# Optimization experiments

Hardware: AMD Instinct MI355X
Metric: run time of the kernel (lower is better)

The kernel has to match this reference:

```python
import jax, jax.numpy as jnp
import numpy as np

BS, P, R, D = 32, 128, 16, 1024
RHO = 0.97
EPS = 1e-8


def unit_normalize(x):
    return x / jnp.maximum(jnp.linalg.norm(x, axis=-1, keepdims=True), EPS)


def setup_inputs() -> dict:
    key = jax.random.key(0)
    ks = jax.random.split(key, 12)
    scale = 1.0 / np.sqrt(D)
    return {
        "x_all": jax.random.normal(ks[0], (BS, P, D), jnp.float32),
        "h_all": jax.random.normal(ks[1], (BS, P, D), jnp.float32),
        "surprise_all": jax.random.uniform(ks[2], (BS, P, 1), jnp.float32) * 8.0,
        "reset_mask": jax.random.bernoulli(ks[3], 0.05, (BS, P)),
        "pm_K": unit_normalize(jax.random.normal(ks[4], (BS, R, D), jnp.float32)),
        "pm_V": unit_normalize(jax.random.normal(ks[5], (BS, R, D), jnp.float32)),
        "pm_a": jax.random.uniform(ks[6], (BS, R), jnp.float32),
        "elig_K0": jnp.zeros((BS, R, D), jnp.float32),
        "elig_V0": jnp.zeros((BS, R, D), jnp.float32),
        "W_k": jax.random.normal(ks[7], (D, D), jnp.float32) * scale,
        "b_k": jnp.zeros((D,), jnp.float32),
        "W_v": jax.random.normal(ks[8], (D, D), jnp.float32) * scale,
        "b_v": jnp.zeros((D,), jnp.float32),
    }


def reference(x_all, h_all, surprise_all, reset_mask, pm_K, pm_V, pm_a,
              elig_K0, elig_V0, W_k, b_k, W_v, b_v):
    # ---- apply_batch: read-only slot-memory readout over P tokens ----
    x_q = unit_normalize(x_all)                                  # [BS,P,D]
    scores = jnp.einsum('brd,bpd->bpr', pm_K, x_q)               # [BS,P,R]
    weighted = pm_a[:, None, :] * scores                         # [BS,P,R]
    y_pm = jnp.einsum('bpr,brd->bpd', weighted, pm_V)            # [BS,P,D]

    # ---- update_eligibility_batch: affine scan over P tokens ----
    k_cand = unit_normalize(jnp.einsum('bpd,de->bpe', x_all, W_k) + b_k)  # [BS,P,D]
    v_cand = jnp.einsum('bpd,de->bpe', h_all, W_v) + b_v                  # [BS,P,D]
    gate = jnp.clip(surprise_all[..., 0] / 5.0, 0.0, 1.0)                 # [BS,P]
    a_keep = RHO * (1.0 - reset_mask.astype(jnp.float32))                 # [BS,P]

    def step(carry, inp):
        eK, eV = carry                      # each [BS,R,D]
        k, v, g, a = inp                    # [BS,D],[BS,D],[BS],[BS]
        # b_t = gate * cand, broadcast across the R slots (matches torch expand)
        eK = a[:, None, None] * eK + (g[:, None] * k)[:, None, :]
        eV = a[:, None, None] * eV + (g[:, None] * v)[:, None, :]
        return (eK, eV), None

    xs = (jnp.swapaxes(k_cand, 0, 1), jnp.swapaxes(v_cand, 0, 1),
          gate.T, a_keep.T)                 # leading axis = P
    (elig_K, elig_V), _ = jax.lax.scan(step, (elig_K0, elig_V0), xs)

    return y_pm, elig_K, elig_V
```

## Files before the change

kernel.cpp:

```cpp
#include <hip/hip_runtime.h>
#include <cstdint>
#include <cstddef>

#define NB 32
#define NP 128
#define NR 16
#define ND 1024
#define RHOC 0.97f
#define EPSN 1e-8f

typedef short bf16x8 __attribute__((ext_vector_type(8)));
typedef float f32x4 __attribute__((ext_vector_type(4)));
typedef unsigned short u16x8 __attribute__((ext_vector_type(8)));
typedef unsigned short ushort_t;

__device__ inline ushort_t f2bf(float f) {
  unsigned u = __float_as_uint(f);
  unsigned r = (u + 0x7fffu + ((u >> 16) & 1u)) >> 16;
  return (ushort_t)r;
}
__device__ inline float bf2f(ushort_t v) {
  return __uint_as_float(((unsigned)v) << 16);
}
__device__ inline void gload16(const void* g, void* l) {
  __builtin_amdgcn_global_load_lds(
      (const __attribute__((address_space(1))) void*)g,
      (__attribute__((address_space(3))) void*)l, 16, 0, 0);
}

__global__ __launch_bounds__(256) void prep_kernel(
    const float* __restrict__ surprise, const void* __restrict__ mask,
    const float* __restrict__ x, const float* __restrict__ Wk,
    const float* __restrict__ pmK,
    float* __restrict__ c, float* __restrict__ Abuf, float* __restrict__ csum,
    ushort_t* __restrict__ Xb, float* __restrict__ xnorm,
    ushort_t* __restrict__ WkT, ushort_t* __restrict__ pmKb) {
  __shared__ __align__(16) char smem[8448];
  int bid = blockIdx.x;
  int t = threadIdx.x;
  if (bid < NB) {
    float* a_sh = (float*)smem;
    float* suf  = a_sh + 128;
    float* redc = suf + 129;
    int*   isu8 = (int*)(redc + 128);
    int b = bid;
    if (t == 0) *isu8 = 0;
    __syncthreads();
    const unsigned char* mb = (const unsigned char*)mask;
    int v = 0;
    for (int i = t; i < NB * NP; i += 256)
      if ((i & 3) != 0 && mb[i] != 0) v = 1;
    if (v) *isu8 = 1;
    __syncthreads();
    int u8 = *isu8;
    if (t < NP) {
      int mv = u8 ? mb[b * NP + t] : ((const int*)mask)[b * NP + t];
      a_sh[t] = RHOC * (mv ? 0.f : 1.f);
    }
    __syncthreads();
    if (t == 0) {
      float p = 1.f;
      suf[NP] = 1.f;
      for (int s = NP - 1; s >= 0; --s) { p *= a_sh[s]; suf[s] = p; }
    }
    __syncthreads();
    if (t < NP) {
      float g = fminf(fmaxf(surprise[b * NP + t] * 0.2f, 0.f), 1.f);
      float cv = g * suf[t + 1];
      c[b * NP + t] = cv;
      redc[t] = cv;
    }
    __syncthreads();
    for (int off = 64; off > 0; off >>= 1) {
      if (t < off) redc[t] += redc[t + off];
      __syncthreads();
    }
    if (t == 0) { csum[b] = redc[0]; Abuf[b] = suf[0]; }
  } else if (bid < NB + NB * NP) {
    int row = bid - NB;
    float* red = (float*)smem;
    float4 vv = *(const float4*)&x[(size_t)row * ND + t * 4];
    ushort4 o;
    o.x = f2bf(vv.x); o.y = f2bf(vv.y); o.z = f2bf(vv.z); o.w = f2bf(vv.w);
    *(ushort4*)&Xb[(size_t)row * ND + t * 4] = o;
    float ss = vv.x * vv.x + vv.y * vv.y + vv.z * vv.z + vv.w * vv.w;
#pragma unroll
    for (int off = 32; off > 0; off >>= 1) ss += __shfl_xor(ss, off);
    int wave = t >> 6, lane = t & 63;
    if (lane == 0) red[wave] = ss;
    __syncthreads();
    if (t == 0) xnorm[row] = sqrtf(red[0] + red[1] + red[2] + red[3]);
  } else if (bid < NB + NB * NP + 256) {
    int id2 = bid - (NB + NB * NP);
    ushort_t (*tt)[65] = (ushort_t(*)[65])smem;
    int k0 = (id2 >> 4) * 64, n0 = (id2 & 15) * 64;
#pragma unroll
    for (int i = 0; i < 16; ++i) {
      int r = i * 4 + (t >> 6), cc = t & 63;
      tt[r][cc] = f2bf(Wk[(size_t)(k0 + r) * ND + n0 + cc]);
    }
    __syncthreads();
#pragma unroll
    for (int i = 0; i < 16; ++i) {
      int r = i * 4 + (t >> 6), cc = t & 63;
      WkT[(size_t)(n0 + r) * ND + k0 + cc] = tt[cc][r];
    }
  } else {
    int id3 = bid - (NB + NB * NP + 256);
    size_t base = (size_t)id3 * 2048 + t * 8;
    float4 a = *(const float4*)&pmK[base];
    float4 bq = *(const float4*)&pmK[base + 4];
    u16x8 o;
    o[0] = f2bf(a.x); o[1] = f2bf(a.y); o[2] = f2bf(a.z); o[3] = f2bf(a.w);
    o[4] = f2bf(bq.x); o[5] = f2bf(bq.y); o[6] = f2bf(bq.z); o[7] = f2bf(bq.w);
    *(u16x8*)&pmKb[base] = o;
  }
}

__global__ __launch_bounds__(256, 3) void main_kernel(
    const ushort_t* __restrict__ Xb, const ushort_t* __restrict__ WkT,
    const float* __restrict__ bk, float* __restrict__ norms2p,
    const float* __restrict__ h, const float* __restrict__ c,
    float* __restrict__ hbar) {
  __shared__ __align__(16) char smem[50176];
  int bid = blockIdx.x;
  int tid = threadIdx.x;
  int grp = bid >> 3, sub = bid & 7;
  int id = (grp >> 1) * 8 + sub;
  if ((grp & 1) == 0) {
    ushort_t* As = (ushort_t*)smem;
    ushort_t* Bs = As + 2 * 128 * 64;
    float* sred = (float*)(Bs + 2 * 64 * 64);
    int lane = tid & 63, wid = tid >> 6;
    int wr = wid >> 1, wc = wid & 1;
    int bm = id & 31, bn = id >> 5;
    int m0 = bm * 128, n0 = bn * 64;
    int lo = lane & 15, hi = lane >> 4;
    f32x4 acc[4][2] = {};

    int ra = tid >> 1, sa = (tid & 1) * 4;
#define STAGE(buf, k0)                                                        \
  {                                                                           \
    _Pragma("unroll") for (int i = 0; i < 4; ++i) {                           \
      int sl = i * 256 + tid;                                                 \
      int r = sl >> 3, s = sl & 7;                                            \
      int gk = (k0) + ((s ^ (r & 7)) << 3);                                   \
      gload16(&Xb[(size_t)(m0 + r) * ND + gk],                                \
              &As[(size_t)(buf)*8192 + ((size_t)sl << 3)]);                   \
    }                                                                         \
    _Pragma("unroll") for (int i = 0; i < 2; ++i) {                           \
      int sl = i * 256 + tid;                                                 \
      int r = sl >> 3, s = sl & 7;                                            \
      int gk = (k0) + ((s ^ (r & 7)) << 3);                                   \
      gload16(&WkT[(size_t)(n0 + r) * ND + gk],                               \
              &Bs[(size_t)(buf)*4096 + ((size_t)sl << 3)]);                   \
    }                                                                         \
  }

    STAGE(0, 0);
    __syncthreads();
    int cur = 0;
    for (int t = 0; t < 16; ++t) {
      if (t < 15) STAGE(cur ^ 1, (t + 1) * 64);
      const ushort_t* Ab = As + cur * 8192;
      const ushort_t* Bb = Bs + cur * 4096;
#pragma unroll
      for (int ksl = 0; ksl < 2; ++ksl) {
        bf16x8 af[4], bfr[2];
#pragma unroll
        for (int mi = 0; mi < 4; ++mi) {
          int r = wr * 64 + mi * 16 + lo;
          int s = (ksl * 4 + hi) ^ (r & 7);
          af[mi] = *(const bf16x8*)&Ab[(r << 6) + (s << 3)];
        }
#pragma unroll
        for (int ni = 0; ni < 2; ++ni) {
          int r = wc * 32 + ni * 16 + lo;
          int s = (ksl * 4 + hi) ^ (r & 7);
          bfr[ni] = *(const bf16x8*)&Bb[(r << 6) + (s << 3)];
        }
#pragma unroll
        for (int mi = 0; mi < 4; ++mi)
#pragma unroll
          for (int ni = 0; ni < 2; ++ni)
            acc[mi][ni] = __builtin_amdgcn_mfma_f32_16x16x32_bf16(
                af[mi], bfr[ni], acc[mi][ni], 0, 0, 0);
      }
      __syncthreads();
      cur ^= 1;
    }
#undef STAGE
    float bkv[2];
#pragma unroll
    for (int ni = 0; ni < 2; ++ni) bkv[ni] = bk[n0 + wc * 32 + ni * 16 + lo];
#pragma unroll
    for (int mi = 0; mi < 4; ++mi) {
#pragma unroll
      for (int j = 0; j < 4; ++j) {
        float ss = 0.f;
#pragma unroll
        for (int ni = 0; ni < 2; ++ni) {
          float vv = acc[mi][ni][j] + bkv[ni];
          ss += vv * vv;
        }
        ss += __shfl_xor(ss, 1);
        ss += __shfl_xor(ss, 2);
        ss += __shfl_xor(ss, 4);
        ss += __shfl_xor(ss, 8);
        if (lo == 0) sred[wc * 128 + wr * 64 + mi * 16 + hi * 4 + j] = ss;
      }
    }
    __syncthreads();
    if (tid < 128)
      norms2p[(size_t)bn * (NB * NP) + m0 + tid] = sred[tid] + sred[128 + tid];
  } else {
    int b = id >> 4, dchunk = id & 15;
    float* cs = (float*)smem;
    float* red = cs + 128;
    int dd = tid & 63, sl = tid >> 6;
    int d = dchunk * 64 + dd;
    if (tid < NP) cs[tid] = c[b * NP + tid];
    __syncthreads();
    const float* hb = h + ((size_t)b * NP + sl * 32) * ND + d;
    float acc = 0.f;
#pragma unroll
    for (int tt2 = 0; tt2 < 32; ++tt2) acc += cs[sl * 32 + tt2] * hb[(size_t)tt2 * ND];
    red[sl * 64 + dd] = acc;
    __syncthreads();
    if (sl == 0)
      hbar[(size_t)b * ND + d] = red[dd] + red[64 + dd] + red[128 + dd] + red[192 + dd];
  }
}

__global__ __launch_bounds__(256) void mid_kernel(
    const ushort_t* __restrict__ Xb, const float* __restrict__ norms2p,
    const float* __restrict__ c, float* __restrict__ xbar,
    float* __restrict__ wsum, const ushort_t* __restrict__ pmKb,
    const float* __restrict__ pmV, const float* __restrict__ pma,
    const float* __restrict__ xnorm, float* __restrict__ y) {
  __shared__ __align__(16) char smem[5504];
  int bid = blockIdx.x;
  int tid = threadIdx.x;
  int grp = bid >> 3, sub = bid & 7;
  int id = (grp >> 1) * 8 + sub;
  if ((grp & 1) == 0) {
    float* wsh = (float*)smem;
    float* red = wsh + NP;
    int b = id >> 3;
    int dd = tid & 63, sl = tid >> 6;
    int d = (id & 7) * 128 + dd * 2;
    if (tid < NP) {
      float s = 0.f;
#pragma unroll
      for (int pc = 0; pc < 16; ++pc)
        s += norms2p[(size_t)pc * (NB * NP) + b * NP + tid];
      wsh[tid] = c[b * NP + tid] / fmaxf(sqrtf(s), EPSN);
    }
    __syncthreads();
    if ((id & 7) == 0 && tid == 0) {
      float s = 0.f;
      for (int t2 = 0; t2 < NP; ++t2) s += wsh[t2];
      wsum[b] = s;
    }
    const ushort_t* xb = Xb + ((size_t)b * NP + sl * 32) * ND + d;
    float ax = 0.f, ay = 0.f;
#pragma unroll
    for (int t2 = 0; t2 < 32; ++t2) {
      unsigned u = *(const unsigned*)&xb[(size_t)t2 * ND];
      float w = wsh[sl * 32 + t2];
      ax += w * bf2f((ushort_t)(u & 0xffffu));
      ay += w * bf2f((ushort_t)(u >> 16));
    }
    red[(sl * 64 + dd) * 2 + 0] = ax;
    red[(sl * 64 + dd) * 2 + 1] = ay;
    __syncthreads();
    if (sl == 0) {
      float2 o;
      o.x = red[dd * 2] + red[(64 + dd) * 2] + red[(128 + dd) * 2] + red[(192 + dd) * 2];
      o.y = red[dd * 2 + 1] + red[(64 + dd) * 2 + 1] + red[(128 + dd) * 2 + 1] +
            red[(192 + dd) * 2 + 1];
      *(float2*)&xbar[(size_t)b * ND + d] = o;
    }
  } else {
    int b = id >> 3, p0 = (id & 7) * 16;
    float* sredp = (float*)smem;
    float* wls = sredp + 4 * 16 * 17;
    int lane = tid & 63, wid = tid >> 6;
    int lo = lane & 15, hi = lane >> 4;
    float4 v[16];
#pragma unroll
    for (int r = 0; r < 16; ++r)
      v[r] = *(const float4*)&pmV[((size_t)(b * NR + r)) * ND + tid * 4];
    const ushort_t* xrow = &Xb[((size_t)(b * NP + p0 + lo)) * ND];
    const ushort_t* krow = &pmKb[((size_t)(b * NR + lo)) * ND];
    f32x4 sc = {};
#pragma unroll
    for (int ki = 0; ki < 8; ++ki) {
      int koff = (wid * 8 + ki) * 32 + hi * 8;
      bf16x8 af = *(const bf16x8*)&xrow[koff];
      bf16x8 bf = *(const bf16x8*)&krow[koff];
      sc = __builtin_amdgcn_mfma_f32_16x16x32_bf16(af, bf, sc, 0, 0, 0);
    }
#pragma unroll
    for (int j = 0; j < 4; ++j) sredp[(wid * 16 + hi * 4 + j) * 17 + lo] = sc[j];
    __syncthreads();
    {
      int p = tid >> 4, r = tid & 15;
      float s = sredp[(p)*17 + r] + sredp[(16 + p) * 17 + r] +
                sredp[(32 + p) * 17 + r] + sredp[(48 + p) * 17 + r];
      wls[p * 16 + r] = pma[b * NR + r] * s / fmaxf(xnorm[b * NP + p0 + p], EPSN);
    }
    __syncthreads();
#pragma unroll
    for (int p = 0; p < 16; ++p) {
      float4 a = {0.f, 0.f, 0.f, 0.f};
#pragma unroll
      for (int r = 0; r < 16; ++r) {
        float w = wls[p * 16 + r];
        a.x += w * v[r].x; a.y += w * v[r].y;
        a.z += w * v[r].z; a.w += w * v[r].w;
      }
      *(float4*)&y[((size_t)(b * NP + p0 + p)) * ND + tid * 4] = a;
    }
  }
}

__global__ __launch_bounds__(256) void vkbar_kernel(
    const float* __restrict__ hbar, const float* __restrict__ xbar,
    const float* __restrict__ Wv, const float* __restrict__ Wk,
    float* __restrict__ partials) {
  __shared__ __align__(16) float hst[128][36];
  int bid = blockIdx.x;
  int path = bid >> 7;
  int id2 = bid & 127;
  int esl = id2 >> 4, dchunk = id2 & 15;
  int e0 = esl * 128, d0 = dchunk * 64;
  const float* src = path ? xbar : hbar;
  const float* W = path ? Wk : Wv;
  int t = threadIdx.x;
#pragma unroll
  for (int i = 0; i < 16; ++i) {
    int idx = i * 256 + t;
    int bb = idx >> 7, e = idx & 127;
    hst[e][bb] = src[(size_t)bb * ND + e0 + e];
  }
  __syncthreads();
  int bg = t >> 6, dd = t & 63, d = d0 + dd;
  float acc[8] = {};
  for (int e = 0; e < 128; ++e) {
    float w = W[(size_t)(e0 + e) * ND + d];
    float4 h0 = *(const float4*)&hst[e][bg * 8];
    float4 h1 = *(const float4*)&hst[e][bg * 8 + 4];
    acc[0] += h0.x * w; acc[1] += h0.y * w; acc[2] += h0.z * w; acc[3] += h0.w * w;
    acc[4] += h1.x * w; acc[5] += h1.y * w; acc[6] += h1.z * w; acc[7] += h1.w * w;
  }
#pragma unroll
  for (int i = 0; i < 8; ++i)
    partials[((size_t)(path * 8 + esl) * NB + bg * 8 + i) * ND + d] = acc[i];
}

__global__ __launch_bounds__(256) void epi_kernel(
    const float* __restrict__ partials, const float* __restrict__ bv,
    const float* __restrict__ bk, const float* __restrict__ eV0,
    const float* __restrict__ eK0, const float* __restrict__ Abuf,
    const float* __restrict__ csum, const float* __restrict__ wsum,
    float* __restrict__ outV, float* __restrict__ outK) {
  int bid = blockIdx.x;
  int path = bid >> 7;
  int id2 = bid & 127;
  int b = id2 >> 2, dc = id2 & 3;
  int d = dc * 256 + threadIdx.x;
  float s = 0.f;
#pragma unroll
  for (int sl = 0; sl < 8; ++sl)
    s += partials[((size_t)(path * 8 + sl) * NB + b) * ND + d];
  const float* bias = path ? bk : bv;
  const float* coef = path ? wsum : csum;
  const float* e0p = path ? eK0 : eV0;
  float* out = path ? outK : outV;
  s += coef[b] * bias[d];
  float A = Abuf[b];
#pragma unroll
  for (int r = 0; r < NR; ++r) {
    size_t idx = ((size_t)(b * NR + r)) * ND + d;
    out[idx] = A * e0p[idx] + s;
  }
}

extern "C" void kernel_launch(void* const* d_in, const int* in_sizes, int n_in,
                              void* d_out, int out_size, void* d_ws, size_t ws_size,
                              hipStream_t stream) {
  (void)in_sizes; (void)n_in; (void)out_size; (void)ws_size;
  const float* x_all    = (const float*)d_in[0];
  const float* h_all    = (const float*)d_in[1];
  const float* surprise = (const float*)d_in[2];
  const void*  mask     = d_in[3];
  const float* pmK      = (const float*)d_in[4];
  const float* pmV      = (const float*)d_in[5];
  const float* pma      = (const float*)d_in[6];
  const float* eK0      = (const float*)d_in[7];
  const float* eV0      = (const float*)d_in[8];
  const float* Wk       = (const float*)d_in[9];
  const float* bk       = (const float*)d_in[10];
  const float* Wv       = (const float*)d_in[11];
  const float* bv       = (const float*)d_in[12];

  float* y    = (float*)d_out;
  float* outK = y + (size_t)NB * NP * ND;
  float* outV = outK + (size_t)NB * NR * ND;

  char* w = (char*)d_ws;
  float* c        = (float*)w; w += NB * NP * 4;
  float* Abuf     = (float*)w; w += 256;
  float* csum     = (float*)w; w += 256;
  float* wsum     = (float*)w; w += 256;
  float* hbar     = (float*)w; w += NB * ND * 4;
  float* xbar     = (float*)w; w += NB * ND * 4;
  float* norms2p  = (float*)w; w += (size_t)16 * NB * NP * 4;
  float* xnorm    = (float*)w; w += NB * NP * 4;
  float* partials = (float*)w; w += (size_t)16 * NB * ND * 4;
  ushort_t* WkT   = (ushort_t*)w; w += (size_t)ND * ND * 2;
  ushort_t* pmKb  = (ushort_t*)w; w += (size_t)NB * NR * ND * 2;
  ushort_t* Xb    = (ushort_t*)w; w += (size_t)NB * NP * ND * 2;

  prep_kernel<<<NB + NB * NP + 256 + 256, 256, 0, stream>>>(
      surprise, mask, x_all, Wk, pmK, c, Abuf, csum, Xb, xnorm, WkT, pmKb);
  main_kernel<<<512 + 512, 256, 0, stream>>>(Xb, WkT, bk, norms2p, h_all, c, hbar);
  mid_kernel<<<256 + 256, 256, 0, stream>>>(Xb, norms2p, c, xbar, wsum, pmKb,
                                            pmV, pma, xnorm, y);
  vkbar_kernel<<<256, 256, 0, stream>>>(hbar, xbar, Wv, Wk, partials);
  epi_kernel<<<256, 256, 0, stream>>>(partials, bv, bk, eV0, eK0, Abuf, csum,
                                      wsum, outV, outK);
}
```

Baseline: 66.69 us.

## Reschedule work across kernels and fuse matvec with eligibility epilogue

The hbar reduction (c-weighted sum of h) moves into prep_kernel, and each of its blocks recomputes the decay suffix products locally. The y readout moves into main_kernel alongside the Wk GEMM. The Wv/Wk matvecs are fused with the eligibility epilogue into d3/d4 kernels, which drops the partials buffer and one launch. The aim is better load balance and fewer launches and global round trips, at the cost of redundant mask/suffix work per block and a less parallel matvec (2 batches per block over the full e range).

```diff
diff --git a/kernel.cpp b/kernel.cpp
--- a/kernel.cpp
+++ b/kernel.cpp
@@ -31,22 +31,23 @@
 __global__ __launch_bounds__(256) void prep_kernel(
     const float* __restrict__ surprise, const void* __restrict__ mask,
     const float* __restrict__ x, const float* __restrict__ Wk,
-    const float* __restrict__ pmK,
+    const float* __restrict__ pmK, const float* __restrict__ h,
     float* __restrict__ c, float* __restrict__ Abuf, float* __restrict__ csum,
     ushort_t* __restrict__ Xb, float* __restrict__ xnorm,
-    ushort_t* __restrict__ WkT, ushort_t* __restrict__ pmKb) {
+    ushort_t* __restrict__ WkT, ushort_t* __restrict__ pmKb,
+    float* __restrict__ hbar) {
   __shared__ __align__(16) char smem[8448];
   int bid = blockIdx.x;
   int t = threadIdx.x;
+  const unsigned char* mb = (const unsigned char*)mask;
   if (bid < NB) {
     float* a_sh = (float*)smem;
     float* suf  = a_sh + 128;
-    float* redc = suf + 129;
+    float* redc = suf + 132;
     int*   isu8 = (int*)(redc + 128);
     int b = bid;
     if (t == 0) *isu8 = 0;
     __syncthreads();
-    const unsigned char* mb = (const unsigned char*)mask;
     int v = 0;
     for (int i = t; i < NB * NP; i += 256)
       if ((i & 3) != 0 && mb[i] != 0) v = 1;
@@ -76,8 +77,51 @@
       __syncthreads();
     }
     if (t == 0) { csum[b] = redc[0]; Abuf[b] = suf[0]; }
-  } else if (bid < NB + NB * NP) {
-    int row = bid - NB;
+  } else if (bid < NB + 512) {
+    int id = bid - NB;
+    int b = id >> 4, dchunk = id & 15;
+    float* asw = (float*)smem;
+    float* suf = asw + 128;
+    float* cs  = suf + 132;
+    float* red = cs + 128;
+    int* isu8  = (int*)(red + 256);
+    if (t == 0) *isu8 = 0;
+    __syncthreads();
+    int v = 0;
+    for (int i = t; i < NB * NP; i += 256)
+      if ((i & 3) != 0 && mb[i] != 0) v = 1;
+    if (v) *isu8 = 1;
+    __syncthreads();
+    int u8 = *isu8;
+    if (t < NP) {
+      int mv = u8 ? mb[b * NP + t] : ((const int*)mask)[b * NP + t];
+      asw[t] = RHOC * (mv ? 0.f : 1.f);
+    }
+    __syncthreads();
+    if (t == 0) {
+      float p = 1.f;
+      suf[NP] = 1.f;
+      for (int s = NP - 1; s >= 0; --s) { p *= asw[s]; suf[s] = p; }
+    }
+    __syncthreads();
+    if (t < NP) {
+      float g = fminf(fmaxf(surprise[b * NP + t] * 0.2f, 0.f), 1.f);
+      cs[t] = g * suf[t + 1];
+    }
+    __syncthreads();
+    int dd = t & 63, sl = t >> 6;
+    int d = dchunk * 64 + dd;
+    const float* hb = h + ((size_t)b * NP + sl * 32) * ND + d;
+    float acc = 0.f;
+#pragma unroll
+    for (int tt2 = 0; tt2 < 32; ++tt2)
+      acc += cs[sl * 32 + tt2] * hb[(size_t)tt2 * ND];
+    red[sl * 64 + dd] = acc;
+    __syncthreads();
+    if (sl == 0)
+      hbar[(size_t)b * ND + d] = red[dd] + red[64 + dd] + red[128 + dd] + red[192 + dd];
+  } else if (bid < NB + 512 + NB * NP) {
+    int row = bid - (NB + 512);
     float* red = (float*)smem;
     float4 vv = *(const float4*)&x[(size_t)row * ND + t * 4];
     ushort4 o;
@@ -90,8 +134,8 @@
     if (lane == 0) red[wave] = ss;
     __syncthreads();
     if (t == 0) xnorm[row] = sqrtf(red[0] + red[1] + red[2] + red[3]);
-  } else if (bid < NB + NB * NP + 256) {
-    int id2 = bid - (NB + NB * NP);
+  } else if (bid < NB + 512 + NB * NP + 256) {
+    int id2 = bid - (NB + 512 + NB * NP);
     ushort_t (*tt)[65] = (ushort_t(*)[65])smem;
     int k0 = (id2 >> 4) * 64, n0 = (id2 & 15) * 64;
 #pragma unroll
@@ -106,7 +150,7 @@
       WkT[(size_t)(n0 + r) * ND + k0 + cc] = tt[cc][r];
     }
   } else {
-    int id3 = bid - (NB + NB * NP + 256);
+    int id3 = bid - (NB + 512 + NB * NP + 256);
     size_t base = (size_t)id3 * 2048 + t * 8;
     float4 a = *(const float4*)&pmK[base];
     float4 bq = *(const float4*)&pmK[base + 4];
@@ -120,25 +164,23 @@
 __global__ __launch_bounds__(256, 3) void main_kernel(
     const ushort_t* __restrict__ Xb, const ushort_t* __restrict__ WkT,
     const float* __restrict__ bk, float* __restrict__ norms2p,
-    const float* __restrict__ h, const float* __restrict__ c,
-    float* __restrict__ hbar) {
+    const ushort_t* __restrict__ pmKb, const float* __restrict__ pmV,
+    const float* __restrict__ pma, const float* __restrict__ xnorm,
+    float* __restrict__ y) {
   __shared__ __align__(16) char smem[50176];
   int bid = blockIdx.x;
   int tid = threadIdx.x;
-  int grp = bid >> 3, sub = bid & 7;
-  int id = (grp >> 1) * 8 + sub;
-  if ((grp & 1) == 0) {
+  if (bid < 512) {
     ushort_t* As = (ushort_t*)smem;
     ushort_t* Bs = As + 2 * 128 * 64;
     float* sred = (float*)(Bs + 2 * 64 * 64);
     int lane = tid & 63, wid = tid >> 6;
     int wr = wid >> 1, wc = wid & 1;
-    int bm = id & 31, bn = id >> 5;
+    int bm = bid & 31, bn = bid >> 5;
     int m0 = bm * 128, n0 = bn * 64;
     int lo = lane & 15, hi = lane >> 4;
     f32x4 acc[4][2] = {};
 
-    int ra = tid >> 1, sa = (tid & 1) * 4;
 #define STAGE(buf, k0)                                                        \
   {                                                                           \
     _Pragma("unroll") for (int i = 0; i < 4; ++i) {                           \
@@ -214,36 +256,109 @@
     if (tid < 128)
       norms2p[(size_t)bn * (NB * NP) + m0 + tid] = sred[tid] + sred[128 + tid];
   } else {
-    int b = id >> 4, dchunk = id & 15;
-    float* cs = (float*)smem;
-    float* red = cs + 128;
-    int dd = tid & 63, sl = tid >> 6;
-    int d = dchunk * 64 + dd;
-    if (tid < NP) cs[tid] = c[b * NP + tid];
-    __syncthreads();
-    const float* hb = h + ((size_t)b * NP + sl * 32) * ND + d;
-    float acc = 0.f;
-#pragma unroll
-    for (int tt2 = 0; tt2 < 32; ++tt2) acc += cs[sl * 32 + tt2] * hb[(size_t)tt2 * ND];
-    red[sl * 64 + dd] = acc;
-    __syncthreads();
-    if (sl == 0)
-      hbar[(size_t)b * ND + d] = red[dd] + red[64 + dd] + red[128 + dd] + red[192 + dd];
-  }
-}
-
-__global__ __launch_bounds__(256) void mid_kernel(
+    int id2 = bid - 512;
+    int b = id2 >> 3, p0 = (id2 & 7) * 16;
+    float* sredp = (float*)smem;
+    float* wls = sredp + 4 * 16 * 17;
+    int lane = tid & 63, wid = tid >> 6;
+    int lo = lane & 15, hi = lane >> 4;
+    float4 v[16];
+#pragma unroll
+    for (int r = 0; r < 16; ++r)
+      v[r] = *(const float4*)&pmV[((size_t)(b * NR + r)) * ND + tid * 4];
+    const ushort_t* xrow = &Xb[((size_t)(b * NP + p0 + lo)) * ND];
+    const ushort_t* krow = &pmKb[((size_t)(b * NR + lo)) * ND];
+    f32x4 sc = {};
+#pragma unroll
+    for (int ki = 0; ki < 8; ++ki) {
+      int koff = (wid * 8 + ki) * 32 + hi * 8;
+      bf16x8 af = *(const bf16x8*)&xrow[koff];
+      bf16x8 bf = *(const bf16x8*)&krow[koff];
+      sc = __builtin_amdgcn_mfma_f32_16x16x32_bf16(af, bf, sc, 0, 0, 0);
+    }
+#pragma unroll
+    for (int j = 0; j < 4; ++j) sredp[(wid * 16 + hi * 4 + j) * 17 + lo] = sc[j];
+    __syncthreads();
+    {
+      int p = tid >> 4, r = tid & 15;
+      float s = sredp[(p)*17 + r] + sredp[(16 + p) * 17 + r] +
+                sredp[(32 + p) * 17 + r] + sredp[(48 + p) * 17 + r];
+      wls[p * 16 + r] = pma[b * NR + r] * s / fmaxf(xnorm[b * NP + p0 + p], EPSN);
+    }
+    __syncthreads();
+#pragma unroll
+    for (int p = 0; p < 16; ++p) {
+      float4 a = {0.f, 0.f, 0.f, 0.f};
+#pragma unroll
+      for (int r = 0; r < 16; ++r) {
+        float w = wls[p * 16 + r];
+        a.x += w * v[r].x; a.y += w * v[r].y;
+        a.z += w * v[r].z; a.w += w * v[r].w;
+      }
+      *(float4*)&y[((size_t)(b * NP + p0 + p)) * ND + tid * 4] = a;
+    }
+  }
+}
+
+__device__ __forceinline__ void eligout_body(
+    int id, int tid, const float* __restrict__ src, const float* __restrict__ W,
+    const float* __restrict__ bias, const float* __restrict__ coef,
+    const float* __restrict__ e0, const float* __restrict__ Abuf,
+    float* __restrict__ out, char* smemv) {
+  int bg = id >> 4, dchunk = id & 15;
+  int b0 = bg * 2;
+  float* hs = (float*)smemv;
+  float* red = hs + 2 * ND;
+  for (int i = tid; i < 2 * ND; i += 256) {
+    int bb = i >> 10, e = i & 1023;
+    hs[bb * ND + e] = src[(size_t)(b0 + bb) * ND + e];
+  }
+  __syncthreads();
+  int esl = tid >> 6, dd = tid & 63;
+  int d = dchunk * 64 + dd;
+  float a0 = 0.f, a1 = 0.f;
+  const float* wcol = W + d;
+#pragma unroll 8
+  for (int ei = 0; ei < 256; ++ei) {
+    int e = esl * 256 + ei;
+    float w = wcol[(size_t)e * ND];
+    a0 += hs[e] * w;
+    a1 += hs[ND + e] * w;
+  }
+  red[(esl * 64 + dd) * 2 + 0] = a0;
+  red[(esl * 64 + dd) * 2 + 1] = a1;
+  __syncthreads();
+  if (tid < 128) {
+    int bb = tid >> 6, dd2 = tid & 63;
+    int d2 = dchunk * 64 + dd2;
+    float s = red[dd2 * 2 + bb] + red[(64 + dd2) * 2 + bb] +
+              red[(128 + dd2) * 2 + bb] + red[(192 + dd2) * 2 + bb];
+    int b = b0 + bb;
+    s += coef[b] * bias[d2];
+    float A = Abuf[b];
+#pragma unroll
+    for (int r = 0; r < NR; ++r) {
+      size_t idx = ((size_t)(b * NR + r)) * ND + d2;
+      out[idx] = A * e0[idx] + s;
+    }
+  }
+}
+
+__global__ __launch_bounds__(256) void d3_kernel(
+    const float* __restrict__ hbar, const float* __restrict__ Wv,
+    const float* __restrict__ bv, const float* __restrict__ csum,
+    const float* __restrict__ eV0, const float* __restrict__ Abuf,
+    float* __restrict__ outV,
     const ushort_t* __restrict__ Xb, const float* __restrict__ norms2p,
     const float* __restrict__ c, float* __restrict__ xbar,
-    float* __restrict__ wsum, const ushort_t* __restrict__ pmKb,
-    const float* __restrict__ pmV, const float* __restrict__ pma,
-    const float* __restrict__ xnorm, float* __restrict__ y) {
-  __shared__ __align__(16) char smem[5504];
+    float* __restrict__ wsum) {
+  __shared__ __align__(16) char smem[10240];
   int bid = blockIdx.x;
   int tid = threadIdx.x;
-  int grp = bid >> 3, sub = bid & 7;
-  int id = (grp >> 1) * 8 + sub;
-  if ((grp & 1) == 0) {
+  if (bid < 256) {
+    eligout_body(bid, tid, hbar, Wv, bv, csum, eV0, Abuf, outV, smem);
+  } else {
+    int id = bid - 256;
     float* wsh = (float*)smem;
     float* red = wsh + NP;
     int b = id >> 3;
@@ -281,110 +396,16 @@
             red[(192 + dd) * 2 + 1];
       *(float2*)&xbar[(size_t)b * ND + d] = o;
     }
-  } else {
-    int b = id >> 3, p0 = (id & 7) * 16;
-    float* sredp = (float*)smem;
-    float* wls = sredp + 4 * 16 * 17;
-    int lane = tid & 63, wid = tid >> 6;
-    int lo = lane & 15, hi = lane >> 4;
-    float4 v[16];
-#pragma unroll
-    for (int r = 0; r < 16; ++r)
-      v[r] = *(const float4*)&pmV[((size_t)(b * NR + r)) * ND + tid * 4];
-    const ushort_t* xrow = &Xb[((size_t)(b * NP + p0 + lo)) * ND];
-    const ushort_t* krow = &pmKb[((size_t)(b * NR + lo)) * ND];
-    f32x4 sc = {};
-#pragma unroll
-    for (int ki = 0; ki < 8; ++ki) {
-      int koff = (wid * 8 + ki) * 32 + hi * 8;
-      bf16x8 af = *(const bf16x8*)&xrow[koff];
-      bf16x8 bf = *(const bf16x8*)&krow[koff];
-      sc = __builtin_amdgcn_mfma_f32_16x16x32_bf16(af, bf, sc, 0, 0, 0);
-    }
-#pragma unroll
-    for (int j = 0; j < 4; ++j) sredp[(wid * 16 + hi * 4 + j) * 17 + lo] = sc[j];
-    __syncthreads();
-    {
-      int p = tid >> 4, r = tid & 15;
-      float s = sredp[(p)*17 + r] + sredp[(16 + p) * 17 + r] +
-                sredp[(32 + p) * 17 + r] + sredp[(48 + p) * 17 + r];
-      wls[p * 16 + r] = pma[b * NR + r] * s / fmaxf(xnorm[b * NP + p0 + p], EPSN);
-    }
-    __syncthreads();
-#pragma unroll
-    for (int p = 0; p < 16; ++p) {
-      float4 a = {0.f, 0.f, 0.f, 0.f};
-#pragma unroll
-      for (int r = 0; r < 16; ++r) {
-        float w = wls[p * 16 + r];
-        a.x += w * v[r].x; a.y += w * v[r].y;
-        a.z += w * v[r].z; a.w += w * v[r].w;
-      }
-      *(float4*)&y[((size_t)(b * NP + p0 + p)) * ND + tid * 4] = a;
-    }
-  }
-}
-
-__global__ __launch_bounds__(256) void vkbar_kernel(
-    const float* __restrict__ hbar, const float* __restrict__ xbar,
-    const float* __restrict__ Wv, const float* __restrict__ Wk,
-    float* __restrict__ partials) {
-  __shared__ __align__(16) float hst[128][36];
-  int bid = blockIdx.x;
-  int path = bid >> 7;
-  int id2 = bid & 127;
-  int esl = id2 >> 4, dchunk = id2 & 15;
-  int e0 = esl * 128, d0 = dchunk * 64;
-  const float* src = path ? xbar : hbar;
-  const float* W = path ? Wk : Wv;
-  int t = threadIdx.x;
-#pragma unroll
-  for (int i = 0; i < 16; ++i) {
-    int idx = i * 256 + t;
-    int bb = idx >> 7, e = idx & 127;
-    hst[e][bb] = src[(size_t)bb * ND + e0 + e];
-  }
-  __syncthreads();
-  int bg = t >> 6, dd = t & 63, d = d0 + dd;
-  float acc[8] = {};
-  for (int e = 0; e < 128; ++e) {
-    float w = W[(size_t)(e0 + e) * ND + d];
-    float4 h0 = *(const float4*)&hst[e][bg * 8];
-    float4 h1 = *(const float4*)&hst[e][bg * 8 + 4];
-    acc[0] += h0.x * w; acc[1] += h0.y * w; acc[2] += h0.z * w; acc[3] += h0.w * w;
-    acc[4] += h1.x * w; acc[5] += h1.y * w; acc[6] += h1.z * w; acc[7] += h1.w * w;
-  }
-#pragma unroll
-  for (int i = 0; i < 8; ++i)
-    partials[((size_t)(path * 8 + esl) * NB + bg * 8 + i) * ND + d] = acc[i];
-}
-
-__global__ __launch_bounds__(256) void epi_kernel(
-    const float* __restrict__ partials, const float* __restrict__ bv,
-    const float* __restrict__ bk, const float* __restrict__ eV0,
+  }
+}
+
+__global__ __launch_bounds__(256) void d4_kernel(
+    const float* __restrict__ xbar, const float* __restrict__ Wk,
+    const float* __restrict__ bk, const float* __restrict__ wsum,
     const float* __restrict__ eK0, const float* __restrict__ Abuf,
-    const float* __restrict__ csum, const float* __restrict__ wsum,
-    float* __restrict__ outV, float* __restrict__ outK) {
-  int bid = blockIdx.x;
-  int path = bid >> 7;
-  int id2 = bid & 127;
-  int b = id2 >> 2, dc = id2 & 3;
-  int d = dc * 256 + threadIdx.x;
-  float s = 0.f;
-#pragma unroll
-  for (int sl = 0; sl < 8; ++sl)
-    s += partials[((size_t)(path * 8 + sl) * NB + b) * ND + d];
-  const float* bias = path ? bk : bv;
-  const float* coef = path ? wsum : csum;
-  const float* e0p = path ? eK0 : eV0;
-  float* out = path ? outK : outV;
-  s += coef[b] * bias[d];
-  float A = Abuf[b];
-#pragma unroll
-  for (int r = 0; r < NR; ++r) {
-    size_t idx = ((size_t)(b * NR + r)) * ND + d;
-    out[idx] = A * e0p[idx] + s;
-  }
+    float* __restrict__ outK) {
+  __shared__ __align__(16) char smem[10240];
+  eligout_body(blockIdx.x, threadIdx.x, xbar, Wk, bk, wsum, eK0, Abuf, outK, smem);
 }
 
 extern "C" void kernel_launch(void* const* d_in, const int* in_sizes, int n_in,
@@ -418,17 +439,16 @@
   float* xbar     = (float*)w; w += NB * ND * 4;
   float* norms2p  = (float*)w; w += (size_t)16 * NB * NP * 4;
   float* xnorm    = (float*)w; w += NB * NP * 4;
-  float* partials = (float*)w; w += (size_t)16 * NB * ND * 4;
   ushort_t* WkT   = (ushort_t*)w; w += (size_t)ND * ND * 2;
   ushort_t* pmKb  = (ushort_t*)w; w += (size_t)NB * NR * ND * 2;
   ushort_t* Xb    = (ushort_t*)w; w += (size_t)NB * NP * ND * 2;
 
-  prep_kernel<<<NB + NB * NP + 256 + 256, 256, 0, stream>>>(
-      surprise, mask, x_all, Wk, pmK, c, Abuf, csum, Xb, xnorm, WkT, pmKb);
-  main_kernel<<<512 + 512, 256, 0, stream>>>(Xb, WkT, bk, norms2p, h_all, c, hbar);
-  mid_kernel<<<256 + 256, 256, 0, stream>>>(Xb, norms2p, c, xbar, wsum, pmKb,
-                                            pmV, pma, xnorm, y);
-  vkbar_kernel<<<256, 256, 0, stream>>>(hbar, xbar, Wv, Wk, partials);
-  epi_kernel<<<256, 256, 0, stream>>>(partials, bv, bk, eV0, eK0, Abuf, csum,
-                                      wsum, outV, outK);
-}
+  prep_kernel<<<NB + 512 + NB * NP + 256 + 256, 256, 0, stream>>>(
+      surprise, mask, x_all, Wk, pmK, h_all, c, Abuf, csum, Xb, xnorm, WkT,
+      pmKb, hbar);
+  main_kernel<<<512 + 256, 256, 0, stream>>>(Xb, WkT, bk, norms2p, pmKb, pmV,
+                                             pma, xnorm, y);
+  d3_kernel<<<256 + 256, 256, 0, stream>>>(hbar, Wv, bv, csum, eV0, Abuf, outV,
+                                           Xb, norms2p, c, xbar, wsum);
+  d4_kernel<<<256, 256, 0, stream>>>(xbar, Wk, bk, wsum, eK0, Abuf, outK);
+}
```

Measured after the change: 66.26 us. No clear change (-0.6%).
